# Optimization experiments

Hardware: AMD Instinct MI355X
Metric: run time of the kernel (lower is better)

The kernel has to match this reference:

```python
import jax, jax.numpy as jnp
import numpy as np

HQ, HK, DH = 32, 8, 64
ROPE_BASE = 10000.0


def _rope_tables(T, dtype):
    pos = jnp.arange(T, dtype=jnp.float32)
    inv_freq = 1.0 / (ROPE_BASE ** (jnp.arange(0, DH, 2, dtype=jnp.float32) / DH))
    freqs = pos[:, None] * inv_freq[None, :]          # (T, DH/2)
    cos = jnp.concatenate([jnp.cos(freqs), jnp.cos(freqs)], -1).astype(dtype)  # (T, DH)
    sin = jnp.concatenate([jnp.sin(freqs), jnp.sin(freqs)], -1).astype(dtype)
    return cos, sin


def _rotate_half(t):
    return jnp.concatenate([-t[..., DH // 2:], t[..., :DH // 2]], -1)


def setup_inputs() -> dict:
    key = jax.random.key(0)
    k1, k2, k3, k4 = jax.random.split(key, 4)
    B, T, D = 2, 2048, 2048
    std = 0.02 / np.sqrt(24)
    kv_std = std / np.sqrt(HQ / HK)
    return {
        "x": jax.random.normal(k1, (B, T, D), jnp.float32),
        "Wq": jax.random.normal(k2, (D, HQ * DH), jnp.float32) * std,
        "Wkv": jax.random.normal(k3, (D, 2 * HK * DH), jnp.float32) * kv_std,
        "Wo": jax.random.normal(k4, (HQ * DH, D), jnp.float32) * std,
    }


def reference(x, Wq, Wkv, Wo):
    B, T, D = x.shape
    g = HQ // HK
    scale = DH ** -0.5
    # projections
    q = (x @ Wq).reshape(B, T, HQ, DH).transpose(0, 2, 1, 3)       # (B,Hq,T,Dh)
    kv = (x @ Wkv).reshape(B, T, 2, HK, DH)
    k = kv[:, :, 0].transpose(0, 2, 1, 3)                           # (B,Hk,T,Dh)
    v = kv[:, :, 1].transpose(0, 2, 1, 3)
    # GQA expand: each kv head repeated g times consecutively
    k = jnp.repeat(k, g, axis=1)                                    # (B,Hq,T,Dh)
    v = jnp.repeat(v, g, axis=1)
    # RoPE on q and repeated k
    cos, sin = _rope_tables(T, x.dtype)
    q = q * cos + _rotate_half(q) * sin
    k = k * cos + _rotate_half(k) * sin
    # attention
    scores = jnp.einsum('bhqd,bhkd->bhqk', q, k) * scale            # (B,Hq,T,T)
    causal = jnp.triu(jnp.ones((T, T), bool), 1)
    scores = jnp.where(causal, -jnp.inf, scores)
    attn = jax.nn.softmax(scores.astype(jnp.float32), axis=-1).astype(x.dtype)
    out = jnp.einsum('bhqk,bhkd->bhqd', attn, v)                    # (B,Hq,T,Dh)
    out = out.transpose(0, 2, 1, 3).reshape(B, T, HQ * DH)
    return out @ Wo
```

## Files before the change

kernel.cpp:

```cpp
#include <hip/hip_runtime.h>
#include <hip/hip_bf16.h>

#define DEVI __device__ __forceinline__

typedef __attribute__((ext_vector_type(4))) float f32x4;
typedef __attribute__((ext_vector_type(16))) float f32x16;
typedef __attribute__((ext_vector_type(8))) short s16x8;
typedef __attribute__((ext_vector_type(4))) short s16x4;
typedef __attribute__((ext_vector_type(2))) unsigned u32x2;

DEVI ushort f2bf(float f) {
  union { float f; unsigned u; } v; v.f = f;
  unsigned r = v.u + 0x7FFFu + ((v.u >> 16) & 1u);
  return (ushort)(r >> 16);
}

DEVI void gload_lds16(const void* g, void* l) {
  __builtin_amdgcn_global_load_lds((const __attribute__((address_space(1))) void*)g,
                                   (__attribute__((address_space(3))) void*)l, 16, 0, 0);
}

#define MFMA16 __builtin_amdgcn_mfma_f32_16x16x32_bf16
#define SBAR() __builtin_amdgcn_s_barrier()
#define LGKM0() asm volatile("s_waitcnt lgkmcnt(0)")

DEVI float plswap_max(float x) {
  union { float f; unsigned u; } a; a.f = x;
  u32x2 r = __builtin_amdgcn_permlane32_swap(a.u, a.u, false, false);
  union { unsigned u; float f; } o0, o1; o0.u = r[0]; o1.u = r[1];
  return fmaxf(o0.f, o1.f);
}
DEVI float plswap_sum(float x) {
  union { float f; unsigned u; } a; a.f = x;
  u32x2 r = __builtin_amdgcn_permlane32_swap(a.u, a.u, false, false);
  union { unsigned u; float f; } o0, o1; o0.u = r[0]; o1.u = r[1];
  return o0.f + o1.f;
}

DEVI void stage128q(const ushort* __restrict__ gsrc, int K, ushort* ld, int tid) {
  #pragma unroll
  for (int j = 0; j < 4; ++j) {
    const int ci = j * 256 + tid;
    const int row = ci >> 3, c = ci & 7;
    gload_lds16(gsrc + (size_t)row * K + ((c ^ (row & 7)) << 3),
                ld + (size_t)(j * 256 + (tid & ~63)) * 8);
  }
}
DEVI s16x8 ldfrag(const ushort* tile, int row, int kc) {
  return *(const s16x8*)((const char*)tile + row * 128 + ((kc ^ (row & 7)) << 4));
}

DEVI void kloop3(const ushort* __restrict__ A, const ushort* __restrict__ BT,
                 ushort* Asm, ushort* Bsm, int m0, int n0, int K, int NKT,
                 f32x4 (&acc)[4][4], int tid, int wm, int wn, int g, int l15) {
  stage128q(A + (size_t)m0 * K, K, Asm, tid);
  stage128q(BT + (size_t)n0 * K, K, Bsm, tid);
  stage128q(BT + (size_t)n0 * K + 64, K, Bsm + 8192, tid);
  asm volatile("s_waitcnt vmcnt(4)");
  SBAR();

  int rd = 0;
  #pragma unroll 1
  for (int t = 0; t < NKT; ++t) {
    const ushort* Ah = Asm + (t & 1) * 8192;
    const ushort* Bh = Bsm + rd * 8192;
    s16x8 af[4][2], bfr[4][2];

    #pragma unroll
    for (int ks = 0; ks < 2; ++ks) {
      #pragma unroll
      for (int ni = 0; ni < 4; ++ni)
        bfr[ni][ks] = ldfrag(Bh, wn * 64 + ni * 16 + l15, ks * 4 + g);
      #pragma unroll
      for (int mi = 0; mi < 4; ++mi)
        af[mi][ks] = ldfrag(Ah, wm * 64 + mi * 16 + l15, ks * 4 + g);
    }
    if (t + 1 < NKT)
      stage128q(A + (size_t)m0 * K + (t + 1) * 64, K, Asm + ((t + 1) & 1) * 8192, tid);
    int wr = rd + 2; if (wr >= 3) wr -= 3;
    if (t + 2 < NKT)
      stage128q(BT + (size_t)n0 * K + (t + 2) * 64, K, Bsm + wr * 8192, tid);

    LGKM0();
    __builtin_amdgcn_sched_barrier(0);
    __builtin_amdgcn_s_setprio(1);
    #pragma unroll
    for (int mi = 0; mi < 4; ++mi)
      #pragma unroll
      for (int ni = 0; ni < 2; ++ni)
        #pragma unroll
        for (int ks = 0; ks < 2; ++ks)
          acc[mi][ni] = MFMA16(af[mi][ks], bfr[ni][ks], acc[mi][ni], 0, 0, 0);
    #pragma unroll
    for (int mi = 0; mi < 4; ++mi)
      #pragma unroll
      for (int ni = 0; ni < 2; ++ni)
        #pragma unroll
        for (int ks = 0; ks < 2; ++ks)
          acc[mi][2 + ni] = MFMA16(af[mi][ks], bfr[2 + ni][ks], acc[mi][2 + ni], 0, 0, 0);
    __builtin_amdgcn_s_setprio(0);

    if (t + 2 < NKT)      asm volatile("s_waitcnt vmcnt(4)");
    else if (t + 1 < NKT) asm volatile("s_waitcnt vmcnt(0)");
    SBAR();
    rd = (rd == 2) ? 0 : rd + 1;
  }
}

__global__ __launch_bounds__(256) void preamble_k(const float* __restrict__ x,
                                                  const float* __restrict__ Wq,
                                                  const float* __restrict__ Wkv,
                                                  const float* __restrict__ Wo,
                                                  ushort* __restrict__ xb,
                                                  ushort* __restrict__ WqkvT,
                                                  ushort* __restrict__ WoT,
                                                  float2* __restrict__ tab) {
  const int id = blockIdx.x;
  const int tid = threadIdx.x;

  if (id >= 2560) {
    if (id < 10752) {
      const int lid = id - 2560;
      int i = (lid * 256 + tid) * 4;
      float4 v = *(const float4*)(x + i);
      ushort4 o;
      o.x = f2bf(v.x); o.y = f2bf(v.y); o.z = f2bf(v.z); o.w = f2bf(v.w);
      *(ushort4*)(xb + i) = o;
    } else {
      const int lid = id - 10752;
      int idx = lid * 256 + tid;
      int t = idx >> 5, i = idx & 31;
      float inv = expf(-(float)i * 0.28782313662425575f);
      float ang = (float)t * inv;
      tab[idx] = make_float2(cosf(ang), sinf(ang));
    }
    return;
  }

  __shared__ ushort tile[64][66];
  const float* in; ushort* out; int R, C, bx, by;
  if (id < 1024)        { in = Wq;  out = WqkvT;              R = 2048; C = 2048; bx = id & 31;          by = id >> 5; }
  else if (id < 1536)   { in = Wkv; out = WqkvT + 2048*2048;  R = 2048; C = 1024; bx = (id-1024) & 15;   by = (id-1024) >> 4; }
  else                  { in = Wo;  out = WoT;                R = 2048; C = 2048; bx = (id-1536) & 31;   by = (id-1536) >> 5; }
  const int r0 = by * 64, c0 = bx * 64;
  #pragma unroll
  for (int j = 0; j < 16; ++j) {
    int idx = j * 256 + tid;
    int r = idx >> 6, c = idx & 63;
    tile[c][r] = f2bf(in[(size_t)(r0 + r) * C + c0 + c]);
  }
  __syncthreads();
  #pragma unroll
  for (int j = 0; j < 16; ++j) {
    int idx = j * 256 + tid;
    int c = idx >> 6, r = idx & 63;
    out[(size_t)(c0 + c) * R + r0 + r] = tile[c][r];
  }
}

__global__ __launch_bounds__(256) void gemm_qkv_3b(const ushort* __restrict__ A,
                                                   const ushort* __restrict__ BT,
                                                   const float2* __restrict__ tab,
                                                   ushort* __restrict__ Qp,
                                                   ushort* __restrict__ Kp,
                                                   ushort* __restrict__ Vp) {
  constexpr int K = 2048, NKT = 32;
  __shared__ __attribute__((aligned(128))) ushort smem[40960];
  ushort* Asm = smem;
  ushort* Bsm = smem + 16384;
  ushort* Ot = smem;

  const int tid = threadIdx.x;
  const int ln = tid & 63, wv = tid >> 6;
  const int g = ln >> 4, l15 = ln & 15, l31 = ln & 31, hi = ln >> 5;
  const int wm = wv >> 1, wn = wv & 1;
  const int m0 = blockIdx.y * 128, n0 = blockIdx.x * 128;

  f32x4 acc[4][4];
  #pragma unroll
  for (int i = 0; i < 4; ++i)
    #pragma unroll
    for (int j = 0; j < 4; ++j) acc[i][j] = (f32x4){0.f, 0.f, 0.f, 0.f};

  kloop3(A, BT, Asm, Bsm, m0, n0, K, NKT, acc, tid, wm, wn, g, l15);

  __syncthreads();
  const int bq = m0 >> 11;
  const int tg0 = m0 & 2047;
  const int type = (n0 < 2048) ? 0 : (n0 < 2560 ? 1 : 2);

  #pragma unroll
  for (int mi = 0; mi < 4; ++mi)
    #pragma unroll
    for (int r = 0; r < 4; ++r) {
      const int tl = wm * 64 + mi * 16 + g * 4 + r;
      const int t = tg0 + tl;
      #pragma unroll
      for (int ni = 0; ni < 4; ++ni) {
        const int cl = wn * 64 + ni * 16 + l15;
        float val = acc[mi][ni][r];
        float outv;
        if (type < 2) {
          float pairv = acc[mi][ni ^ 2][r];
          float2 cs = tab[t * 32 + (ni & 1) * 16 + l15];
          outv = (ni & 2) ? (val * cs.x + pairv * cs.y) : (val * cs.x - pairv * cs.y);
          if (type == 0) outv *= 0.18033688011112042f;
        } else {
          outv = val;
        }
        Ot[tl * 132 + cl] = f2bf(outv);
      }
    }
  __syncthreads();

  #pragma unroll
  for (int it = 0; it < 8; ++it) {
    const int id = wv * 8 + it;
    const int hl = id >> 4, q4 = (id >> 2) & 3, fi = id & 3;
    const int tile = (tg0 >> 5) + q4;
    if (type < 2) {
      const ushort* srow = Ot + (q4 * 32 + l31) * 132 + hl * 64 + fi * 16 + hi * 8;
      union { s16x4 h[2]; s16x8 v; } u;
      u.h[0] = *(const s16x4*)srow;
      u.h[1] = *(const s16x4*)(srow + 4);
      ushort* dst;
      if (type == 0) {
        const int h = (n0 >> 6) + hl;
        dst = Qp + (((size_t)(bq * 32 + h) * 64 + tile) * 4 + fi) * 512 + ln * 8;
      } else {
        const int h = ((n0 - 2048) >> 6) + hl;
        dst = Kp + (((size_t)(bq * 8 + h) * 64 + tile) * 4 + fi) * 512 + ln * 8;
      }
      *(s16x8*)dst = u.v;
    } else {
      const int hk = ((n0 - 2560) >> 6) + hl;
      const int col = hl * 64 + (fi & 1) * 32 + l31;
      const int row0 = q4 * 32 + (fi >> 1) * 16 + hi * 8;
      ushort o[8];
      #pragma unroll
      for (int j = 0; j < 8; ++j) o[j] = Ot[(row0 + j) * 132 + col];
      ushort* dst = Vp + (((size_t)(bq * 8 + hk) * 64 + tile) * 4 + fi) * 512 + ln * 8;
      *(s16x8*)dst = *(const s16x8*)o;
    }
  }
}

__global__ __launch_bounds__(256) void gemm_bt_3b(const ushort* __restrict__ A,
                                                  const ushort* __restrict__ BT,
                                                  float* __restrict__ C, int M, int N, int K) {
  __shared__ __attribute__((aligned(128))) ushort smem[40960];
  ushort* Asm = smem;
  ushort* Bsm = smem + 16384;

  const int tid = threadIdx.x;
  const int ln = tid & 63, wv = tid >> 6;
  const int g = ln >> 4, l15 = ln & 15;
  const int wm = wv >> 1, wn = wv & 1;
  const int m0 = blockIdx.y * 128, n0 = blockIdx.x * 128;
  const int NKT = K / 64;

  f32x4 acc[4][4];
  #pragma unroll
  for (int i = 0; i < 4; ++i)
    #pragma unroll
    for (int j = 0; j < 4; ++j) acc[i][j] = (f32x4){0.f, 0.f, 0.f, 0.f};

  kloop3(A, BT, Asm, Bsm, m0, n0, K, NKT, acc, tid, wm, wn, g, l15);

  #pragma unroll
  for (int mi = 0; mi < 4; ++mi)
    #pragma unroll
    for (int r = 0; r < 4; ++r) {
      int row = m0 + wm * 64 + mi * 16 + g * 4 + r;
      float* crow = C + (size_t)row * N + n0 + wn * 64 + l15;
      #pragma unroll
      for (int ni = 0; ni < 4; ++ni) crow[ni * 16] = acc[mi][ni][r];
    }
}

__global__ __launch_bounds__(64) void attn_k(const ushort* __restrict__ Qp,
                                             const ushort* __restrict__ Kp,
                                             const ushort* __restrict__ Vp,
                                             ushort* __restrict__ O) {
  __shared__ ushort ep[32 * 64];
  const int ln = threadIdx.x & 63;
  const int l31 = ln & 31, hi = ln >> 5;

  const int f = blockIdx.x;
  const int xcd = f & 7, j = f >> 3;
  const int pr = xcd + 8 * (j & 1);
  const int b = pr >> 3, hk = pr & 7;
  const int s = j >> 1;
  const int hq = hk * 4 + (s & 3);
  const int qtile = 63 - (s >> 2);
  const int qw = qtile * 32;
  const int nt = qtile + 1;

  const ushort* Qh    = Qp + ((size_t)(b * 32 + hq)) * (64 * 2048);
  const ushort* Kbase = Kp + ((size_t)(b * 8 + hk)) * (64 * 2048);
  const ushort* Vbase = Vp + ((size_t)(b * 8 + hk)) * (64 * 2048);
  ushort* lds = ep;

  s16x8 qf[4];
  {
    const ushort* qp_ = Qh + (size_t)qtile * 2048 + ln * 8;
    #pragma unroll
    for (int ks = 0; ks < 4; ++ks) qf[ks] = *(const s16x8*)(qp_ + ks * 512);
  }

  f32x16 z16;
  #pragma unroll
  for (int r = 0; r < 16; ++r) z16[r] = 0.f;

  f32x16 oacc[2];
  #pragma unroll
  for (int dt = 0; dt < 2; ++dt)
    #pragma unroll
    for (int r = 0; r < 16; ++r) oacc[dt][r] = 0.f;
  float m = -1e30f, l = 0.f;

  const ushort* kp = Kbase + ln * 8;
  const ushort* vp = Vbase + ln * 8;

  s16x8 kf[4];
  #pragma unroll
  for (int ks = 0; ks < 4; ++ks) kf[ks] = *(const s16x8*)(kp + ks * 512);
  kp += 2048;

  s16x8 vc[4];
  union pfu { unsigned u[4]; s16x8 v; };
  pfu pf0, pf1;

  #pragma unroll 1
  for (int kt = 0; kt < nt; ++kt) {
    if (kt) {
      __builtin_amdgcn_s_setprio(1);
      oacc[0] = __builtin_amdgcn_mfma_f32_32x32x16_bf16(vc[0], pf0.v, oacc[0], 0, 0, 0);
      oacc[1] = __builtin_amdgcn_mfma_f32_32x32x16_bf16(vc[1], pf0.v, oacc[1], 0, 0, 0);
      oacc[0] = __builtin_amdgcn_mfma_f32_32x32x16_bf16(vc[2], pf1.v, oacc[0], 0, 0, 0);
      oacc[1] = __builtin_amdgcn_mfma_f32_32x32x16_bf16(vc[3], pf1.v, oacc[1], 0, 0, 0);
      __builtin_amdgcn_s_setprio(0);
    }
    #pragma unroll
    for (int fi2 = 0; fi2 < 4; ++fi2) vc[fi2] = *(const s16x8*)(vp + fi2 * 512);
    vp += 2048;

    __builtin_amdgcn_s_setprio(1);
    f32x16 sp = __builtin_amdgcn_mfma_f32_32x32x16_bf16(kf[0], qf[0], z16, 0, 0, 0);
    sp = __builtin_amdgcn_mfma_f32_32x32x16_bf16(kf[1], qf[1], sp, 0, 0, 0);
    sp = __builtin_amdgcn_mfma_f32_32x32x16_bf16(kf[2], qf[2], sp, 0, 0, 0);
    sp = __builtin_amdgcn_mfma_f32_32x32x16_bf16(kf[3], qf[3], sp, 0, 0, 0);
    __builtin_amdgcn_s_setprio(0);

    if (kt + 1 < nt) {
      #pragma unroll
      for (int ks = 0; ks < 4; ++ks) kf[ks] = *(const s16x8*)(kp + ks * 512);
      kp += 2048;
    }

    if (kt == qtile) {
      #pragma unroll
      for (int r = 0; r < 16; ++r) {
        int key = (r & 3) + 8 * (r >> 2) + 4 * hi;
        if (key > l31) sp[r] = -1e30f;
      }
    }

    float t0 = fmaxf(fmaxf(sp[0], sp[1]), sp[2]);
    float t1 = fmaxf(fmaxf(sp[3], sp[4]), sp[5]);
    float t2 = fmaxf(fmaxf(sp[6], sp[7]), sp[8]);
    float t3 = fmaxf(fmaxf(sp[9], sp[10]), sp[11]);
    float t4 = fmaxf(fmaxf(sp[12], sp[13]), sp[14]);
    float u0 = fmaxf(fmaxf(t0, t1), t2);
    float u1 = fmaxf(fmaxf(t3, t4), sp[15]);
    float pm = plswap_max(fmaxf(u0, u1));

    if (__any(pm - m > 8.0f)) {
      float mn = fmaxf(m, pm);
      float alpha = __builtin_amdgcn_exp2f(m - mn);
      m = mn;
      l *= alpha;
      #pragma unroll
      for (int dt = 0; dt < 2; ++dt)
        #pragma unroll
        for (int r = 0; r < 16; ++r) oacc[dt][r] *= alpha;
    }

    #pragma unroll
    for (int r = 0; r < 16; ++r) sp[r] = __builtin_amdgcn_exp2f(sp[r] - m);
    {
      float a0 = sp[0] + sp[1], a1 = sp[2] + sp[3], a2 = sp[4] + sp[5], a3 = sp[6] + sp[7];
      float a4 = sp[8] + sp[9], a5 = sp[10] + sp[11], a6 = sp[12] + sp[13], a7 = sp[14] + sp[15];
      float b0 = a0 + a1, b1 = a2 + a3, b2 = a4 + a5, b3 = a6 + a7;
      l += plswap_sum((b0 + b1) + (b2 + b3));
    }

    unsigned cw[8];
    #pragma unroll
    for (int jj = 0; jj < 8; ++jj) {
      union { __hip_bfloat162 h; unsigned u; } pk;
      pk.h = __float22bfloat162_rn(make_float2(sp[2 * jj], sp[2 * jj + 1]));
      cw[jj] = pk.u;
    }
    {
      u32x2 r;
      r = __builtin_amdgcn_permlane32_swap(cw[0], cw[2], false, false);
      pf0.u[0] = r[0]; pf0.u[2] = r[1];
      r = __builtin_amdgcn_permlane32_swap(cw[1], cw[3], false, false);
      pf0.u[1] = r[0]; pf0.u[3] = r[1];
      r = __builtin_amdgcn_permlane32_swap(cw[4], cw[6], false, false);
      pf1.u[0] = r[0]; pf1.u[2] = r[1];
      r = __builtin_amdgcn_permlane32_swap(cw[5], cw[7], false, false);
      pf1.u[1] = r[0]; pf1.u[3] = r[1];
    }
  }

  __builtin_amdgcn_s_setprio(1);
  oacc[0] = __builtin_amdgcn_mfma_f32_32x32x16_bf16(vc[0], pf0.v, oacc[0], 0, 0, 0);
  oacc[1] = __builtin_amdgcn_mfma_f32_32x32x16_bf16(vc[1], pf0.v, oacc[1], 0, 0, 0);
  oacc[0] = __builtin_amdgcn_mfma_f32_32x32x16_bf16(vc[2], pf1.v, oacc[0], 0, 0, 0);
  oacc[1] = __builtin_amdgcn_mfma_f32_32x32x16_bf16(vc[3], pf1.v, oacc[1], 0, 0, 0);
  __builtin_amdgcn_s_setprio(0);

  float invl = 1.0f / l;
  #pragma unroll
  for (int dt = 0; dt < 2; ++dt)
    #pragma unroll
    for (int r = 0; r < 16; ++r) {
      int d = dt * 32 + (r & 3) + 8 * (r >> 2) + 4 * hi;
      int byte = (l31 * 128 + d * 2) ^ ((l31 & 7) << 4);
      *(ushort*)((char*)lds + byte) = f2bf(oacc[dt][r] * invl);
    }
  const int qr = ln >> 1, half = ln & 1;
  #pragma unroll
  for (int jj = 0; jj < 4; ++jj) {
    int byte = (qr * 128 + half * 64 + jj * 16) ^ ((qr & 7) << 4);
    s16x8 vrow = *(const s16x8*)((const char*)lds + byte);
    *(s16x8*)(O + ((size_t)(b * 2048 + qw + qr)) * 2048 + hq * 64 + half * 32 + jj * 8) = vrow;
  }
}

extern "C" void kernel_launch(void* const* d_in, const int* in_sizes, int n_in,
                              void* d_out, int out_size, void* d_ws, size_t ws_size,
                              hipStream_t stream) {
  const float* x   = (const float*)d_in[0];
  const float* Wq  = (const float*)d_in[1];
  const float* Wkv = (const float*)d_in[2];
  const float* Wo  = (const float*)d_in[3];
  float* out = (float*)d_out;

  char* ws = (char*)d_ws;
  ushort* xb     = (ushort*)(ws);
  ushort* WqkvT  = (ushort*)(ws + 16777216);
  ushort* WoT    = (ushort*)(ws + 29360128);
  float2* tab    = (float2*)(ws + 37748736);
  ushort* Qp     = (ushort*)(ws + 38273024);
  ushort* Kp     = (ushort*)(ws + 55050240);
  ushort* Vp     = (ushort*)(ws + 59244544);
  ushort* Ob     = (ushort*)(ws + 63438848);

  preamble_k<<<11008, 256, 0, stream>>>(x, Wq, Wkv, Wo, xb, WqkvT, WoT, tab);
  gemm_qkv_3b<<<dim3(24, 32), 256, 0, stream>>>(xb, WqkvT, tab, Qp, Kp, Vp);
  attn_k<<<4096, 64, 0, stream>>>(Qp, Kp, Vp, Ob);
  gemm_bt_3b<<<dim3(16, 32), 256, 0, stream>>>(Ob, WoT, out, 4096, 2048, 2048);
}
```

Before: 204.1 us.

## Process two GQA query heads per attention wave sharing K/V fragments

Each single-wave attention workgroup now handles two query heads of the same KV group for one query tile. The K and V fragments loaded per key tile are reused across both heads, which halves K/V global traffic and the number of workgroups. The two heads' independent MFMA chains are interleaved to hide latency. In exchange, register pressure roughly doubles, so waves_per_eu is pinned to 2, which limits occupancy and risks exposing load latency.

Result: no change. 200.9 us, median of 2 (-1.6%).

```diff
diff --git a/kernel.cpp b/kernel.cpp
--- a/kernel.cpp
+++ b/kernel.cpp
@@ -21,6 +21,7 @@
 }
 
 #define MFMA16 __builtin_amdgcn_mfma_f32_16x16x32_bf16
+#define MFMA32 __builtin_amdgcn_mfma_f32_32x32x16_bf16
 #define SBAR() __builtin_amdgcn_s_barrier()
 #define LGKM0() asm volatile("s_waitcnt lgkmcnt(0)")
 
@@ -278,11 +279,13 @@
     }
 }
 
-__global__ __launch_bounds__(64) void attn_k(const ushort* __restrict__ Qp,
-                                             const ushort* __restrict__ Kp,
-                                             const ushort* __restrict__ Vp,
-                                             ushort* __restrict__ O) {
-  __shared__ ushort ep[32 * 64];
+__global__ __attribute__((amdgpu_flat_work_group_size(64, 64)))
+__attribute__((amdgpu_waves_per_eu(2, 2)))
+void attn_k(const ushort* __restrict__ Qp,
+            const ushort* __restrict__ Kp,
+            const ushort* __restrict__ Vp,
+            ushort* __restrict__ O) {
+  __shared__ ushort ep[2][32 * 64];
   const int ln = threadIdx.x & 63;
   const int l31 = ln & 31, hi = ln >> 5;
 
@@ -291,33 +294,39 @@
   const int pr = xcd + 8 * (j & 1);
   const int b = pr >> 3, hk = pr & 7;
   const int s = j >> 1;
-  const int hq = hk * 4 + (s & 3);
-  const int qtile = 63 - (s >> 2);
+  const int hp = s & 1;
+  const int hq0 = hk * 4 + hp * 2, hq1 = hq0 + 1;
+  const int qtile = 63 - (s >> 1);
   const int qw = qtile * 32;
   const int nt = qtile + 1;
 
-  const ushort* Qh    = Qp + ((size_t)(b * 32 + hq)) * (64 * 2048);
+  const ushort* QhA   = Qp + ((size_t)(b * 32 + hq0)) * (64 * 2048);
+  const ushort* QhB   = Qp + ((size_t)(b * 32 + hq1)) * (64 * 2048);
   const ushort* Kbase = Kp + ((size_t)(b * 8 + hk)) * (64 * 2048);
   const ushort* Vbase = Vp + ((size_t)(b * 8 + hk)) * (64 * 2048);
-  ushort* lds = ep;
-
-  s16x8 qf[4];
+
+  s16x8 qfA[4], qfB[4];
   {
-    const ushort* qp_ = Qh + (size_t)qtile * 2048 + ln * 8;
-    #pragma unroll
-    for (int ks = 0; ks < 4; ++ks) qf[ks] = *(const s16x8*)(qp_ + ks * 512);
+    const ushort* qa = QhA + (size_t)qtile * 2048 + ln * 8;
+    const ushort* qb = QhB + (size_t)qtile * 2048 + ln * 8;
+    #pragma unroll
+    for (int ks = 0; ks < 4; ++ks) {
+      qfA[ks] = *(const s16x8*)(qa + ks * 512);
+      qfB[ks] = *(const s16x8*)(qb + ks * 512);
+    }
   }
 
   f32x16 z16;
   #pragma unroll
   for (int r = 0; r < 16; ++r) z16[r] = 0.f;
 
-  f32x16 oacc[2];
-  #pragma unroll
-  for (int dt = 0; dt < 2; ++dt)
-    #pragma unroll
-    for (int r = 0; r < 16; ++r) oacc[dt][r] = 0.f;
-  float m = -1e30f, l = 0.f;
+  f32x16 oaccA[2], oaccB[2];
+  #pragma unroll
+  for (int r = 0; r < 16; ++r) {
+    oaccA[0][r] = 0.f; oaccA[1][r] = 0.f;
+    oaccB[0][r] = 0.f; oaccB[1][r] = 0.f;
+  }
+  float mA = -1e30f, lA = 0.f, mB = -1e30f, lB = 0.f;
 
   const ushort* kp = Kbase + ln * 8;
   const ushort* vp = Vbase + ln * 8;
@@ -329,16 +338,20 @@
 
   s16x8 vc[4];
   union pfu { unsigned u[4]; s16x8 v; };
-  pfu pf0, pf1;
+  pfu pfA0, pfA1, pfB0, pfB1;
 
   #pragma unroll 1
   for (int kt = 0; kt < nt; ++kt) {
     if (kt) {
       __builtin_amdgcn_s_setprio(1);
-      oacc[0] = __builtin_amdgcn_mfma_f32_32x32x16_bf16(vc[0], pf0.v, oacc[0], 0, 0, 0);
-      oacc[1] = __builtin_amdgcn_mfma_f32_32x32x16_bf16(vc[1], pf0.v, oacc[1], 0, 0, 0);
-      oacc[0] = __builtin_amdgcn_mfma_f32_32x32x16_bf16(vc[2], pf1.v, oacc[0], 0, 0, 0);
-      oacc[1] = __builtin_amdgcn_mfma_f32_32x32x16_bf16(vc[3], pf1.v, oacc[1], 0, 0, 0);
+      oaccA[0] = MFMA32(vc[0], pfA0.v, oaccA[0], 0, 0, 0);
+      oaccB[0] = MFMA32(vc[0], pfB0.v, oaccB[0], 0, 0, 0);
+      oaccA[1] = MFMA32(vc[1], pfA0.v, oaccA[1], 0, 0, 0);
+      oaccB[1] = MFMA32(vc[1], pfB0.v, oaccB[1], 0, 0, 0);
+      oaccA[0] = MFMA32(vc[2], pfA1.v, oaccA[0], 0, 0, 0);
+      oaccB[0] = MFMA32(vc[2], pfB1.v, oaccB[0], 0, 0, 0);
+      oaccA[1] = MFMA32(vc[3], pfA1.v, oaccA[1], 0, 0, 0);
+      oaccB[1] = MFMA32(vc[3], pfB1.v, oaccB[1], 0, 0, 0);
       __builtin_amdgcn_s_setprio(0);
     }
     #pragma unroll
@@ -346,10 +359,14 @@
     vp += 2048;
 
     __builtin_amdgcn_s_setprio(1);
-    f32x16 sp = __builtin_amdgcn_mfma_f32_32x32x16_bf16(kf[0], qf[0], z16, 0, 0, 0);
-    sp = __builtin_amdgcn_mfma_f32_32x32x16_bf16(kf[1], qf[1], sp, 0, 0, 0);
-    sp = __builtin_amdgcn_mfma_f32_32x32x16_bf16(kf[2], qf[2], sp, 0, 0, 0);
-    sp = __builtin_amdgcn_mfma_f32_32x32x16_bf16(kf[3], qf[3], sp, 0, 0, 0);
+    f32x16 spA = MFMA32(kf[0], qfA[0], z16, 0, 0, 0);
+    f32x16 spB = MFMA32(kf[0], qfB[0], z16, 0, 0, 0);
+    spA = MFMA32(kf[1], qfA[1], spA, 0, 0, 0);
+    spB = MFMA32(kf[1], qfB[1], spB, 0, 0, 0);
+    spA = MFMA32(kf[2], qfA[2], spA, 0, 0, 0);
+    spB = MFMA32(kf[2], qfB[2], spB, 0, 0, 0);
+    spA = MFMA32(kf[3], qfA[3], spA, 0, 0, 0);
+    spB = MFMA32(kf[3], qfB[3], spB, 0, 0, 0);
     __builtin_amdgcn_s_setprio(0);
 
     if (kt + 1 < nt) {
@@ -362,81 +379,132 @@
       #pragma unroll
       for (int r = 0; r < 16; ++r) {
         int key = (r & 3) + 8 * (r >> 2) + 4 * hi;
-        if (key > l31) sp[r] = -1e30f;
+        if (key > l31) { spA[r] = -1e30f; spB[r] = -1e30f; }
       }
     }
 
-    float t0 = fmaxf(fmaxf(sp[0], sp[1]), sp[2]);
-    float t1 = fmaxf(fmaxf(sp[3], sp[4]), sp[5]);
-    float t2 = fmaxf(fmaxf(sp[6], sp[7]), sp[8]);
-    float t3 = fmaxf(fmaxf(sp[9], sp[10]), sp[11]);
-    float t4 = fmaxf(fmaxf(sp[12], sp[13]), sp[14]);
-    float u0 = fmaxf(fmaxf(t0, t1), t2);
-    float u1 = fmaxf(fmaxf(t3, t4), sp[15]);
-    float pm = plswap_max(fmaxf(u0, u1));
-
-    if (__any(pm - m > 8.0f)) {
-      float mn = fmaxf(m, pm);
-      float alpha = __builtin_amdgcn_exp2f(m - mn);
-      m = mn;
-      l *= alpha;
-      #pragma unroll
-      for (int dt = 0; dt < 2; ++dt)
-        #pragma unroll
-        for (int r = 0; r < 16; ++r) oacc[dt][r] *= alpha;
-    }
-
-    #pragma unroll
-    for (int r = 0; r < 16; ++r) sp[r] = __builtin_amdgcn_exp2f(sp[r] - m);
+    float pa, pb;
     {
-      float a0 = sp[0] + sp[1], a1 = sp[2] + sp[3], a2 = sp[4] + sp[5], a3 = sp[6] + sp[7];
-      float a4 = sp[8] + sp[9], a5 = sp[10] + sp[11], a6 = sp[12] + sp[13], a7 = sp[14] + sp[15];
-      float b0 = a0 + a1, b1 = a2 + a3, b2 = a4 + a5, b3 = a6 + a7;
-      l += plswap_sum((b0 + b1) + (b2 + b3));
-    }
-
-    unsigned cw[8];
+      float t0 = fmaxf(fmaxf(spA[0], spA[1]), spA[2]);
+      float t1 = fmaxf(fmaxf(spA[3], spA[4]), spA[5]);
+      float t2 = fmaxf(fmaxf(spA[6], spA[7]), spA[8]);
+      float t3 = fmaxf(fmaxf(spA[9], spA[10]), spA[11]);
+      float t4 = fmaxf(fmaxf(spA[12], spA[13]), spA[14]);
+      pa = plswap_max(fmaxf(fmaxf(fmaxf(t0, t1), t2), fmaxf(fmaxf(t3, t4), spA[15])));
+      float u0 = fmaxf(fmaxf(spB[0], spB[1]), spB[2]);
+      float u1 = fmaxf(fmaxf(spB[3], spB[4]), spB[5]);
+      float u2 = fmaxf(fmaxf(spB[6], spB[7]), spB[8]);
+      float u3 = fmaxf(fmaxf(spB[9], spB[10]), spB[11]);
+      float u4 = fmaxf(fmaxf(spB[12], spB[13]), spB[14]);
+      pb = plswap_max(fmaxf(fmaxf(fmaxf(u0, u1), u2), fmaxf(fmaxf(u3, u4), spB[15])));
+    }
+
+    if (__any(pa - mA > 8.0f)) {
+      float mn = fmaxf(mA, pa);
+      float alpha = __builtin_amdgcn_exp2f(mA - mn);
+      mA = mn; lA *= alpha;
+      #pragma unroll
+      for (int r = 0; r < 16; ++r) { oaccA[0][r] *= alpha; oaccA[1][r] *= alpha; }
+    }
+    if (__any(pb - mB > 8.0f)) {
+      float mn = fmaxf(mB, pb);
+      float alpha = __builtin_amdgcn_exp2f(mB - mn);
+      mB = mn; lB *= alpha;
+      #pragma unroll
+      for (int r = 0; r < 16; ++r) { oaccB[0][r] *= alpha; oaccB[1][r] *= alpha; }
+    }
+
+    #pragma unroll
+    for (int r = 0; r < 16; ++r) {
+      spA[r] = __builtin_amdgcn_exp2f(spA[r] - mA);
+      spB[r] = __builtin_amdgcn_exp2f(spB[r] - mB);
+    }
+    {
+      float a0 = spA[0] + spA[1], a1 = spA[2] + spA[3], a2 = spA[4] + spA[5], a3 = spA[6] + spA[7];
+      float a4 = spA[8] + spA[9], a5 = spA[10] + spA[11], a6 = spA[12] + spA[13], a7 = spA[14] + spA[15];
+      lA += plswap_sum(((a0 + a1) + (a2 + a3)) + ((a4 + a5) + (a6 + a7)));
+      float b0 = spB[0] + spB[1], b1 = spB[2] + spB[3], b2 = spB[4] + spB[5], b3 = spB[6] + spB[7];
+      float b4 = spB[8] + spB[9], b5 = spB[10] + spB[11], b6 = spB[12] + spB[13], b7 = spB[14] + spB[15];
+      lB += plswap_sum(((b0 + b1) + (b2 + b3)) + ((b4 + b5) + (b6 + b7)));
+    }
+
+    unsigned cwA[8], cwB[8];
     #pragma unroll
     for (int jj = 0; jj < 8; ++jj) {
       union { __hip_bfloat162 h; unsigned u; } pk;
-      pk.h = __float22bfloat162_rn(make_float2(sp[2 * jj], sp[2 * jj + 1]));
-      cw[jj] = pk.u;
+      pk.h = __float22bfloat162_rn(make_float2(spA[2 * jj], spA[2 * jj + 1]));
+      cwA[jj] = pk.u;
+      pk.h = __float22bfloat162_rn(make_float2(spB[2 * jj], spB[2 * jj + 1]));
+      cwB[jj] = pk.u;
     }
     {
       u32x2 r;
-      r = __builtin_amdgcn_permlane32_swap(cw[0], cw[2], false, false);
-      pf0.u[0] = r[0]; pf0.u[2] = r[1];
-      r = __builtin_amdgcn_permlane32_swap(cw[1], cw[3], false, false);
-      pf0.u[1] = r[0]; pf0.u[3] = r[1];
-      r = __builtin_amdgcn_permlane32_swap(cw[4], cw[6], false, false);
-      pf1.u[0] = r[0]; pf1.u[2] = r[1];
-      r = __builtin_amdgcn_permlane32_swap(cw[5], cw[7], false, false);
-      pf1.u[1] = r[0]; pf1.u[3] = r[1];
+      r = __builtin_amdgcn_permlane32_swap(cwA[0], cwA[2], false, false);
+      pfA0.u[0] = r[0]; pfA0.u[2] = r[1];
+      r = __builtin_amdgcn_permlane32_swap(cwA[1], cwA[3], false, false);
+      pfA0.u[1] = r[0]; pfA0.u[3] = r[1];
+      r = __builtin_amdgcn_permlane32_swap(cwA[4], cwA[6], false, false);
+      pfA1.u[0] = r[0]; pfA1.u[2] = r[1];
+      r = __builtin_amdgcn_permlane32_swap(cwA[5], cwA[7], false, false);
+      pfA1.u[1] = r[0]; pfA1.u[3] = r[1];
+      r = __builtin_amdgcn_permlane32_swap(cwB[0], cwB[2], false, false);
+      pfB0.u[0] = r[0]; pfB0.u[2] = r[1];
+      r = __builtin_amdgcn_permlane32_swap(cwB[1], cwB[3], false, false);
+      pfB0.u[1] = r[0]; pfB0.u[3] = r[1];
+      r = __builtin_amdgcn_permlane32_swap(cwB[4], cwB[6], false, false);
+      pfB1.u[0] = r[0]; pfB1.u[2] = r[1];
+      r = __builtin_amdgcn_permlane32_swap(cwB[5], cwB[7], false, false);
+      pfB1.u[1] = r[0]; pfB1.u[3] = r[1];
     }
   }
 
   __builtin_amdgcn_s_setprio(1);
-  oacc[0] = __builtin_amdgcn_mfma_f32_32x32x16_bf16(vc[0], pf0.v, oacc[0], 0, 0, 0);
-  oacc[1] = __builtin_amdgcn_mfma_f32_32x32x16_bf16(vc[1], pf0.v, oacc[1], 0, 0, 0);
-  oacc[0] = __builtin_amdgcn_mfma_f32_32x32x16_bf16(vc[2], pf1.v, oacc[0], 0, 0, 0);
-  oacc[1] = __builtin_amdgcn_mfma_f32_32x32x16_bf16(vc[3], pf1.v, oacc[1], 0, 0, 0);
+  oaccA[0] = MFMA32(vc[0], pfA0.v, oaccA[0], 0, 0, 0);
+  oaccB[0] = MFMA32(vc[0], pfB0.v, oaccB[0], 0, 0, 0);
+  oaccA[1] = MFMA32(vc[1], pfA0.v, oaccA[1], 0, 0, 0);
+  oaccB[1] = MFMA32(vc[1], pfB0.v, oaccB[1], 0, 0, 0);
+  oaccA[0] = MFMA32(vc[2], pfA1.v, oaccA[0], 0, 0, 0);
+  oaccB[0] = MFMA32(vc[2], pfB1.v, oaccB[0], 0, 0, 0);
+  oaccA[1] = MFMA32(vc[3], pfA1.v, oaccA[1], 0, 0, 0);
+  oaccB[1] = MFMA32(vc[3], pfB1.v, oaccB[1], 0, 0, 0);
   __builtin_amdgcn_s_setprio(0);
 
-  float invl = 1.0f / l;
-  #pragma unroll
-  for (int dt = 0; dt < 2; ++dt)
-    #pragma unroll
-    for (int r = 0; r < 16; ++r) {
-      int d = dt * 32 + (r & 3) + 8 * (r >> 2) + 4 * hi;
-      int byte = (l31 * 128 + d * 2) ^ ((l31 & 7) << 4);
-      *(ushort*)((char*)lds + byte) = f2bf(oacc[dt][r] * invl);
-    }
   const int qr = ln >> 1, half = ln & 1;
-  #pragma unroll
-  for (int jj = 0; jj < 4; ++jj) {
-    int byte = (qr * 128 + half * 64 + jj * 16) ^ ((qr & 7) << 4);
-    s16x8 vrow = *(const s16x8*)((const char*)lds + byte);
-    *(s16x8*)(O + ((size_t)(b * 2048 + qw + qr)) * 2048 + hq * 64 + half * 32 + jj * 8) = vrow;
+  {
+    float invl = 1.0f / lA;
+    ushort* lds = ep[0];
+    #pragma unroll
+    for (int dt = 0; dt < 2; ++dt)
+      #pragma unroll
+      for (int r = 0; r < 16; ++r) {
+        int d = dt * 32 + (r & 3) + 8 * (r >> 2) + 4 * hi;
+        int byte = (l31 * 128 + d * 2) ^ ((l31 & 7) << 4);
+        *(ushort*)((char*)lds + byte) = f2bf(oaccA[dt][r] * invl);
+      }
+    #pragma unroll
+    for (int jj = 0; jj < 4; ++jj) {
+      int byte = (qr * 128 + half * 64 + jj * 16) ^ ((qr & 7) << 4);
+      s16x8 vrow = *(const s16x8*)((const char*)lds + byte);
+      *(s16x8*)(O + ((size_t)(b * 2048 + qw + qr)) * 2048 + hq0 * 64 + half * 32 + jj * 8) = vrow;
+    }
+  }
+  {
+    float invl = 1.0f / lB;
+    ushort* lds = ep[1];
+    #pragma unroll
+    for (int dt = 0; dt < 2; ++dt)
+      #pragma unroll
+      for (int r = 0; r < 16; ++r) {
+        int d = dt * 32 + (r & 3) + 8 * (r >> 2) + 4 * hi;
+        int byte = (l31 * 128 + d * 2) ^ ((l31 & 7) << 4);
+        *(ushort*)((char*)lds + byte) = f2bf(oaccB[dt][r] * invl);
+      }
+    #pragma unroll
+    for (int jj = 0; jj < 4; ++jj) {
+      int byte = (qr * 128 + half * 64 + jj * 16) ^ ((qr & 7) << 4);
+      s16x8 vrow = *(const s16x8*)((const char*)lds + byte);
+      *(s16x8*)(O + ((size_t)(b * 2048 + qw + qr)) * 2048 + hq1 * 64 + half * 32 + jj * 8) = vrow;
+    }
   }
 }
 
@@ -461,6 +529,6 @@
 
   preamble_k<<<11008, 256, 0, stream>>>(x, Wq, Wkv, Wo, xb, WqkvT, WoT, tab);
   gemm_qkv_3b<<<dim3(24, 32), 256, 0, stream>>>(xb, WqkvT, tab, Qp, Kp, Vp);
-  attn_k<<<4096, 64, 0, stream>>>(Qp, Kp, Vp, Ob);
+  attn_k<<<2048, 64, 0, stream>>>(Qp, Kp, Vp, Ob);
   gemm_bt_3b<<<dim3(16, 32), 256, 0, stream>>>(Ob, WoT, out, 4096, 2048, 2048);
 }
```
